# Kernel optimization log

Hardware: AMD Instinct MI355X
Metric: run time of the kernel (lower is better)

Reference implementation:

```python
import jax, jax.numpy as jnp
import numpy as np

N_HEAD = 8
DROP_RATE = 0.1


def setup_inputs() -> dict:
    key = jax.random.key(0)
    k1, k2, k3 = jax.random.split(key, 3)
    n, c, h, w = 16, 512, 32, 32
    return {
        "x": jax.random.normal(k1, (n, c, h, w), jnp.float32),
        "qkv_w": jax.random.normal(k2, (3 * c, c), jnp.float32) * 0.02,
        "qkv_b": jnp.zeros((3 * c,), jnp.float32),
        "out_w": jax.random.normal(k3, (c, c), jnp.float32) * 0.02,
        "out_b": jnp.zeros((c,), jnp.float32),
        "dropout_enabled": 0,
    }


def reference(x, qkv_w, qkv_b, out_w, out_b, dropout_enabled):
    n, c, h, w = x.shape
    hd = c // N_HEAD  # head dim
    # fused QKV 1x1 conv == per-pixel matmul: [n, 3c, h, w]
    qkv = jnp.einsum('oc,nchw->nohw', qkv_w, x) + qkv_b[None, :, None, None]
    # [n, 3*n_head, hd, h*w] -> [n, 3*n_head, h*w, hd]
    qkv = jnp.swapaxes(qkv.reshape(n, N_HEAD * 3, hd, h * w), 2, 3)
    q, k, v = jnp.split(qkv, 3, axis=1)  # each [n, n_head, hw, hd]
    scale = hd ** (-0.25)
    att = jax.nn.softmax((q * scale) @ (jnp.swapaxes(k, 2, 3) * scale), axis=3)
    y = jnp.swapaxes(att @ v, 2, 3).reshape(n, c, h, w)
    y = jnp.einsum('oc,nchw->nohw', out_w, y) + out_b[None, :, None, None]
    # Dropout2d: drops whole (n, c) channel maps
    rate = DROP_RATE * dropout_enabled
    keep = jax.random.bernoulli(jax.random.key(42), 1.0 - rate, shape=(n, c))
    y = y * keep[..., None, None] / (1.0 - rate)
    return x + y
```

## Files before the change

kernel.cpp:

```cpp
#include <hip/hip_runtime.h>

typedef short bf16x8 __attribute__((ext_vector_type(8)));
typedef float f32x4 __attribute__((ext_vector_type(4)));
typedef float f32x16 __attribute__((ext_vector_type(16)));

#define MFMA16(a,b,c) __builtin_amdgcn_mfma_f32_16x16x32_bf16((a),(b),(c),0,0,0)
#define MFMA32(a,b,c) __builtin_amdgcn_mfma_f32_32x32x16_bf16((a),(b),(c),0,0,0)

static __device__ __forceinline__ unsigned short f2bf(float f){
  unsigned u; __builtin_memcpy(&u, &f, 4);
  u += 0x7fffu + ((u >> 16) & 1u);
  return (unsigned short)(u >> 16);
}

static __device__ __forceinline__ unsigned cvtpk(float lo, float hi){
  unsigned r;
  asm volatile("v_cvt_pk_bf16_f32 %0, %1, %2" : "=v"(r) : "v"(lo), "v"(hi));
  return r;
}
static __device__ __forceinline__ void pl32swap(unsigned &a, unsigned &b){
  asm volatile("v_permlane32_swap_b32 %0, %1" : "+v"(a), "+v"(b));
}

static __device__ __forceinline__ void gload_lds16(const void* g, void* l) {
  __builtin_amdgcn_global_load_lds(
      (__attribute__((address_space(1))) void*)g,
      (__attribute__((address_space(3))) void*)l, 16, 0, 0);
}

__global__ __launch_bounds__(256) void cvt_w(
    const float* __restrict__ qkv_w, const float* __restrict__ out_w,
    unsigned short* __restrict__ wq, unsigned short* __restrict__ wo) {
  int i = blockIdx.x * 256 + threadIdx.x;
  if (i < 786432) wq[i] = f2bf(qkv_w[i]);
  else            wo[i - 786432] = f2bf(out_w[i - 786432]);
}

__global__ __launch_bounds__(256) void transpose_cvt(
    const float* __restrict__ in, unsigned short* __restrict__ out)
{
  __shared__ unsigned short tile[32][33];
  const long base = (long)blockIdx.z * 512 * 1024;
  const int t = threadIdx.x, tx = t & 31, ty = t >> 5;
  const int c0 = blockIdx.x * 32, r0 = blockIdx.y * 32;
  const float* ib = in + base;
#pragma unroll
  for (int i = 0; i < 4; ++i)
    tile[ty + i * 8][tx] = f2bf(ib[(long)(r0 + ty + i * 8) * 1024 + c0 + tx]);
  __syncthreads();
  unsigned short* ob = out + base;
#pragma unroll
  for (int i = 0; i < 4; ++i)
    ob[(long)(c0 + ty + i * 8) * 512 + r0 + tx] = tile[tx][ty + i * 8];
}

__global__ __launch_bounds__(256, 2) void gemm_qkv(
    const unsigned short* __restrict__ A, const unsigned short* __restrict__ B,
    unsigned short* __restrict__ qkvout, const float* __restrict__ bias)
{
  const int M = 1024, K = 512;
  __shared__ unsigned short SM[4][128 * 64];
  const int t = threadIdx.x, lane = t & 63, wv = t >> 6;
  const int quad = lane >> 4, ln = lane & 15;

  const int L = blockIdx.x + 12 * blockIdx.y + 96 * blockIdx.z;
  const int v = (L & 7) * 192 + (L >> 3);
  const int m0 = ((v / 12) & 7) * 128, n0 = (v % 12) * 128;
  const long zb = v / 96;
  A += zb * (long)M * K;

  const int srow = wv * 32 + (lane >> 3);
  const int scol = ((lane & 7) * 8) ^ ((lane >> 3) * 8);

  auto stage = [&](int kt, unsigned short* Ad, unsigned short* Bd) {
#pragma unroll
    for (int i = 0; i < 4; ++i) {
      gload_lds16(&A[(long)(m0 + srow + i * 8) * K + kt + scol],
                  &Ad[(wv * 32 + i * 8) * 64]);
      gload_lds16(&B[(long)(n0 + srow + i * 8) * K + kt + scol],
                  &Bd[(wv * 32 + i * 8) * 64]);
    }
  };

  f32x4 zero = {0.f, 0.f, 0.f, 0.f};
  f32x4 acc[4][4];
#pragma unroll
  for (int i = 0; i < 4; ++i)
#pragma unroll
    for (int j = 0; j < 4; ++j) acc[i][j] = zero;

  const int wm = (wv & 1) * 64, wn = (wv >> 1) * 64;
  const int rsw = (ln & 7) * 8;

  stage(0, SM[0], SM[2]);
  __syncthreads();
  for (int kt8 = 0; kt8 < 8; ++kt8) {
    const int cur = kt8 & 1;
    if (kt8 < 7) stage((kt8 + 1) * 64, SM[cur ^ 1], SM[2 + (cur ^ 1)]);
    const unsigned short* As = SM[cur];
    const unsigned short* Bs = SM[2 + cur];
#pragma unroll
    for (int kk = 0; kk < 64; kk += 32) {
      bf16x8 a[4], b[4];
#pragma unroll
      for (int i = 0; i < 4; ++i)
        a[i] = *(const bf16x8*)&As[(wm + i * 16 + ln) * 64 + ((kk + quad * 8) ^ rsw)];
#pragma unroll
      for (int j = 0; j < 4; ++j)
        b[j] = *(const bf16x8*)&Bs[(wn + j * 16 + ln) * 64 + ((kk + quad * 8) ^ rsw)];
#pragma unroll
      for (int i = 0; i < 4; ++i)
#pragma unroll
        for (int j = 0; j < 4; ++j)
          acc[i][j] = MFMA16(a[i], b[j], acc[i][j]);
    }
    __syncthreads();
  }

  const int part = n0 >> 9;
  if (part < 2) {
    const float qs = (part == 0) ? 0.18033688f : 1.0f;
    unsigned short (*T)[136] = (unsigned short(*)[136])&SM[0][0];
#pragma unroll
    for (int j = 0; j < 4; ++j) {
      const int oo = wn + j * 16 + ln;
      const float bb = bias[n0 + oo];
#pragma unroll
      for (int i = 0; i < 4; ++i) {
        const int pp = wm + i * 16 + quad * 4;
        f32x4 vv = acc[i][j];
#pragma unroll
        for (int r = 0; r < 4; ++r)
          T[pp + r][oo] = f2bf((vv[r] + bb) * qs);
      }
    }
    __syncthreads();
    unsigned short* qb = qkvout + (long)part * 8388608;
#pragma unroll
    for (int it = 0; it < 8; ++it) {
      const int idx = it * 256 + t;
      const int p = idx >> 4, c0 = (idx & 15) * 8;
      const int og = n0 + c0;
      const int h = (og >> 6) & 7, d = og & 63;
      bf16x8 val = *(const bf16x8*)&T[p][c0];
      *(bf16x8*)&qb[((long)(zb * 8 + h) * 1024 + m0 + p) * 64 + d] = val;
    }
  } else {
#pragma unroll
    for (int j = 0; j < 4; ++j) {
      const int o = n0 + wn + j * 16 + ln;
      const float bb = bias[o];
#pragma unroll
      for (int i = 0; i < 4; ++i) {
        const int p = m0 + wm + i * 16 + quad * 4;
        const long cidx = ((long)zb * 512 + (o - 1024)) * 1024 + p;
        f32x4 vv = acc[i][j];
        ushort4 st;
        st.x = f2bf(vv[0] + bb); st.y = f2bf(vv[1] + bb);
        st.z = f2bf(vv[2] + bb); st.w = f2bf(vv[3] + bb);
        *(ushort4*)&qkvout[16777216 + cidx] = st;
      }
    }
  }
}

__global__ __launch_bounds__(256, 2) void gemm_out(
    const unsigned short* __restrict__ A, const unsigned short* __restrict__ B,
    float* __restrict__ C, const float* __restrict__ bias,
    const float* __restrict__ xin, const int* __restrict__ de_ptr)
{
  const int M = 1024, K = 512;
  __shared__ unsigned short SM[4][128 * 64];
  const int t = threadIdx.x, lane = t & 63, wv = t >> 6;
  const int quad = lane >> 4, ln = lane & 15;

  const int L = blockIdx.x + 4 * blockIdx.y + 32 * blockIdx.z;
  const int v = (L & 7) * 64 + (L >> 3);
  const int m0 = ((v >> 2) & 7) * 128, n0 = (v & 3) * 128;
  const long zb = v >> 5;
  A += zb * (long)M * K;
  C += zb * 512l * M;
  xin += zb * 512l * M;

  const int srow = wv * 32 + (lane >> 3);
  const int scol = ((lane & 7) * 8) ^ ((lane >> 3) * 8);

  auto stage = [&](int kt, unsigned short* Ad, unsigned short* Bd) {
#pragma unroll
    for (int i = 0; i < 4; ++i) {
      gload_lds16(&A[(long)(m0 + srow + i * 8) * K + kt + scol],
                  &Ad[(wv * 32 + i * 8) * 64]);
      gload_lds16(&B[(long)(n0 + srow + i * 8) * K + kt + scol],
                  &Bd[(wv * 32 + i * 8) * 64]);
    }
  };

  f32x4 zero = {0.f, 0.f, 0.f, 0.f};
  f32x4 acc[4][4];
#pragma unroll
  for (int i = 0; i < 4; ++i)
#pragma unroll
    for (int j = 0; j < 4; ++j) acc[i][j] = zero;

  const int wm = (wv & 1) * 64, wn = (wv >> 1) * 64;
  const int rsw = (ln & 7) * 8;

  stage(0, SM[0], SM[2]);
  __syncthreads();
  for (int kt8 = 0; kt8 < 8; ++kt8) {
    const int cur = kt8 & 1;
    if (kt8 < 7) stage((kt8 + 1) * 64, SM[cur ^ 1], SM[2 + (cur ^ 1)]);
    const unsigned short* As = SM[cur];
    const unsigned short* Bs = SM[2 + cur];
#pragma unroll
    for (int kk = 0; kk < 64; kk += 32) {
      bf16x8 a[4], b[4];
#pragma unroll
      for (int i = 0; i < 4; ++i)
        a[i] = *(const bf16x8*)&As[(wm + i * 16 + ln) * 64 + ((kk + quad * 8) ^ rsw)];
#pragma unroll
      for (int j = 0; j < 4; ++j)
        b[j] = *(const bf16x8*)&Bs[(wn + j * 16 + ln) * 64 + ((kk + quad * 8) ^ rsw)];
#pragma unroll
      for (int i = 0; i < 4; ++i)
#pragma unroll
        for (int j = 0; j < 4; ++j)
          acc[i][j] = MFMA16(a[i], b[j], acc[i][j]);
    }
    __syncthreads();
  }

  float dscale = 1.0f / (1.0f - 0.1f * (float)de_ptr[0]);

#pragma unroll
  for (int j = 0; j < 4; ++j) {
    int o = n0 + wn + j * 16 + ln;
    float bb = bias[o];
#pragma unroll
    for (int i = 0; i < 4; ++i) {
      int p = m0 + wm + i * 16 + quad * 4;
      long cidx = (long)o * M + p;
      f32x4 vv = acc[i][j];
      float4 rx = *(const float4*)&xin[cidx];
      float4 st;
      st.x = rx.x + (vv[0] + bb) * dscale;
      st.y = rx.y + (vv[1] + bb) * dscale;
      st.z = rx.z + (vv[2] + bb) * dscale;
      st.w = rx.w + (vv[3] + bb) * dscale;
      *(float4*)&C[cidx] = st;
    }
  }
}

__global__ __launch_bounds__(512, 2) void attn_kernel(
    const unsigned short* __restrict__ q_pd, const unsigned short* __restrict__ k_pd,
    const unsigned short* __restrict__ v_cp, unsigned short* __restrict__ y_pc)
{
  __shared__ unsigned short Ks[2][128 * 64];
  __shared__ unsigned short Vs[2][64 * 128];
  const int t = threadIdx.x, lane = t & 63, wv = t >> 6;
  const int l31 = lane & 31, bh8 = (lane >> 5) * 8;
  const int qt = blockIdx.y >> 5;
  const int nh = blockIdx.x * 32 + (blockIdx.y & 31);
  const int n = nh >> 3, h = nh & 7;
  const int q0 = qt * 512;

  bf16x8 qa[2][4];
#pragma unroll
  for (int qg = 0; qg < 2; ++qg) {
    const unsigned short* qb =
        q_pd + ((long)nh * 1024 + q0 + wv * 64 + qg * 32 + l31) * 64;
#pragma unroll
    for (int ds = 0; ds < 4; ++ds)
      qa[qg][ds] = *(const bf16x8*)(qb + ds * 16 + bh8);
  }

  f32x16 zacc;
#pragma unroll
  for (int r = 0; r < 16; ++r) zacc[r] = 0.f;
  f32x16 o_acc[2][2];
  o_acc[0][0] = zacc; o_acc[0][1] = zacc; o_acc[1][0] = zacc; o_acc[1][1] = zacc;
  float l_acc[2] = {0.f, 0.f};

  const unsigned short* kg0 = k_pd + (long)nh * 1024 * 64;
  const unsigned short* vg0 = v_cp + ((long)n * 512 + h * 64) * 1024;

  const int krow = lane >> 3;
  const int kcol = ((lane & 7) * 8) ^ ((lane >> 3) * 8);
  const int vrow = lane >> 4;
  const int rsw = (lane & 7) * 8;
  const int vrsw = (l31 & 15) * 8;

  auto stage_kv = [&](int c, int buf) {
    const unsigned short* kg = kg0 + (long)c * 128 * 64;
    const unsigned short* vg = vg0 + c * 128;
    unsigned short* KsD = Ks[buf];
    unsigned short* VsD = Vs[buf];
#pragma unroll
    for (int i = 0; i < 2; ++i) {
      const int vr = ((wv & 1) * 8) + i * 4 + vrow;
      const int vcol = ((lane & 15) ^ vr) * 8;
      gload_lds16(kg + (long)(wv * 16 + i * 8 + krow) * 64 + kcol,
                  &KsD[(wv * 16 + i * 8) * 64]);
      gload_lds16(vg + (long)(wv * 8 + i * 4 + vrow) * 1024 + vcol,
                  &VsD[(wv * 8 + i * 4) * 128]);
    }
  };

  stage_kv(0, 0);

  union U { bf16x8 v; unsigned u[4]; };
  auto sm_pack = [&](const f32x16& sv, bf16x8* paq, float& lac) {
    float e[16];
#pragma unroll
    for (int r = 0; r < 16; ++r) e[r] = __builtin_amdgcn_exp2f(sv[r]);
    float a0 = e[0] + e[1],  a1 = e[2] + e[3],  a2 = e[4] + e[5],  a3 = e[6] + e[7];
    float a4 = e[8] + e[9],  a5 = e[10] + e[11], a6 = e[12] + e[13], a7 = e[14] + e[15];
    float b0 = a0 + a1, b1 = a2 + a3, b2 = a4 + a5, b3 = a6 + a7;
    lac += (b0 + b1) + (b2 + b3);
    unsigned pk4[4][2];
#pragma unroll
    for (int hh = 0; hh < 4; ++hh) {
      pk4[hh][0] = cvtpk(e[4 * hh + 0], e[4 * hh + 1]);
      pk4[hh][1] = cvtpk(e[4 * hh + 2], e[4 * hh + 3]);
    }
#pragma unroll
    for (int hk = 0; hk < 2; ++hk) {
      unsigned x0 = pk4[2 * hk + 1][0], y0 = pk4[2 * hk][0];
      unsigned x1 = pk4[2 * hk + 1][1], y1 = pk4[2 * hk][1];
      pl32swap(x0, y0); pl32swap(x1, y1);
      U u; u.u[0] = y0; u.u[1] = y1; u.u[2] = x0; u.u[3] = x1;
      paq[hk] = u.v;
    }
  };

  for (int c = 0; c < 8; ++c) {
    const int cur = c & 1;
    if (c < 7) {
      stage_kv(c + 1, cur ^ 1);
      asm volatile("s_waitcnt vmcnt(4)" ::: "memory");
    } else {
      asm volatile("s_waitcnt vmcnt(0)" ::: "memory");
    }
    __builtin_amdgcn_s_barrier();
    const unsigned short* KsC = Ks[cur];
    const unsigned short* VsC = Vs[cur];

#pragma unroll
    for (int g = 0; g < 2; ++g) {
      bf16x8 ka[2][4];
#pragma unroll
      for (int kk = 0; kk < 2; ++kk)
#pragma unroll
        for (int ds = 0; ds < 4; ++ds)
          ka[kk][ds] = *(const bf16x8*)
              &KsC[((g * 2 + kk) * 32 + l31) * 64 + ((ds * 16 + bh8) ^ rsw)];
      f32x16 s[2][2];
      s[0][0] = zacc; s[0][1] = zacc; s[1][0] = zacc; s[1][1] = zacc;
      __builtin_amdgcn_s_setprio(1);
#pragma unroll
      for (int ds = 0; ds < 4; ++ds)
#pragma unroll
        for (int kk = 0; kk < 2; ++kk) {
          s[kk][0] = MFMA32(ka[kk][ds], qa[0][ds], s[kk][0]);
          s[kk][1] = MFMA32(ka[kk][ds], qa[1][ds], s[kk][1]);
        }
      __builtin_amdgcn_s_setprio(0);
#pragma unroll
      for (int kk = 0; kk < 2; ++kk) {
        bf16x8 va[4];
#pragma unroll
        for (int dg = 0; dg < 2; ++dg)
#pragma unroll
          for (int hk = 0; hk < 2; ++hk)
            va[dg * 2 + hk] = *(const bf16x8*)
                &VsC[(dg * 32 + l31) * 128 + ((((g * 2 + kk) * 2 + hk) * 16 + bh8) ^ vrsw)];
        bf16x8 pa[2][2];
        sm_pack(s[kk][0], pa[0], l_acc[0]);
        sm_pack(s[kk][1], pa[1], l_acc[1]);
        __builtin_amdgcn_s_setprio(1);
#pragma unroll
        for (int dg = 0; dg < 2; ++dg)
#pragma unroll
          for (int hk = 0; hk < 2; ++hk) {
            o_acc[dg][0] = MFMA32(va[dg * 2 + hk], pa[0][hk], o_acc[dg][0]);
            o_acc[dg][1] = MFMA32(va[dg * 2 + hk], pa[1][hk], o_acc[dg][1]);
          }
        __builtin_amdgcn_s_setprio(0);
      }
    }
    __builtin_amdgcn_s_barrier();
  }

#pragma unroll
  for (int qg = 0; qg < 2; ++qg) {
    float la = l_acc[qg];
    la += __shfl_xor(la, 32);
    float linv = 1.0f / la;
    const int q = q0 + wv * 64 + qg * 32 + l31;
    unsigned short* yb = y_pc + ((long)n * 1024 + q) * 512 + h * 64;
#pragma unroll
    for (int dg = 0; dg < 2; ++dg) {
      f32x16 o = o_acc[dg][qg];
#pragma unroll
      for (int rq = 0; rq < 4; ++rq) {
        int d0 = dg * 32 + rq * 8 + (bh8 >> 1);
        ushort4 st;
        st.x = f2bf(o[rq * 4 + 0] * linv);
        st.y = f2bf(o[rq * 4 + 1] * linv);
        st.z = f2bf(o[rq * 4 + 2] * linv);
        st.w = f2bf(o[rq * 4 + 3] * linv);
        *(ushort4*)&yb[d0] = st;
      }
    }
  }
}

extern "C" void kernel_launch(void* const* d_in, const int* in_sizes, int n_in,
                              void* d_out, int out_size, void* d_ws, size_t ws_size,
                              hipStream_t stream) {
  (void)in_sizes; (void)n_in; (void)out_size; (void)ws_size;
  const float* x     = (const float*)d_in[0];
  const float* qkv_w = (const float*)d_in[1];
  const float* qkv_b = (const float*)d_in[2];
  const float* out_w = (const float*)d_in[3];
  const float* out_b = (const float*)d_in[4];
  const int* de = (const int*)d_in[5];
  float* out = (float*)d_out;
  unsigned short* ws = (unsigned short*)d_ws;

  unsigned short* xT   = ws;
  unsigned short* qkv  = ws + 8388608;
  unsigned short* y_pc = ws;
  unsigned short* wq   = ws + 33554432;
  unsigned short* wo   = wq + 786432;

  cvt_w<<<4096, 256, 0, stream>>>(qkv_w, out_w, wq, wo);

  transpose_cvt<<<dim3(32, 16, 16), 256, 0, stream>>>(x, xT);

  gemm_qkv<<<dim3(12, 8, 16), 256, 0, stream>>>(xT, wq, qkv, qkv_b);

  attn_kernel<<<dim3(4, 64), 512, 0, stream>>>(
      qkv, qkv + 8388608, qkv + 16777216, y_pc);

  gemm_out<<<dim3(4, 8, 16), 256, 0, stream>>>(
      y_pc, wo, out, out_b, x, de);
}
```

Baseline: 199.8 us.

## Software-pipeline QK and PV MFMAs in attention; fuse weight cvt into transpose

The attention inner loop is restructured so that the QK^T MFMAs for the next 32-key group are issued before the softmax/pack and PV MFMAs of the current group, using ping-pong score registers. This overlaps the softmax VALU work with matrix-core work. Separately, the weight bf16 conversion kernel is merged into the transpose kernel as extra blocks, removing one launch and vectorising the conversion to float2 loads. The pipelining raises register pressure, with two sets of score accumulators live at once.

```diff
diff --git a/kernel.cpp b/kernel.cpp
--- a/kernel.cpp
+++ b/kernel.cpp
@@ -28,18 +28,21 @@
       (__attribute__((address_space(3))) void*)l, 16, 0, 0);
 }
 
-__global__ __launch_bounds__(256) void cvt_w(
+__global__ __launch_bounds__(256) void transpose_cvt(
+    const float* __restrict__ in, unsigned short* __restrict__ out,
     const float* __restrict__ qkv_w, const float* __restrict__ out_w,
-    unsigned short* __restrict__ wq, unsigned short* __restrict__ wo) {
-  int i = blockIdx.x * 256 + threadIdx.x;
-  if (i < 786432) wq[i] = f2bf(qkv_w[i]);
-  else            wo[i - 786432] = f2bf(out_w[i - 786432]);
-}
-
-__global__ __launch_bounds__(256) void transpose_cvt(
-    const float* __restrict__ in, unsigned short* __restrict__ out)
+    unsigned short* __restrict__ wq, unsigned short* __restrict__ wo)
 {
   __shared__ unsigned short tile[32][33];
+  if (blockIdx.x >= 32) {
+    const int b = (blockIdx.x - 32) + 8 * (blockIdx.y + 16 * blockIdx.z);
+    const int i = b * 512 + threadIdx.x * 2;
+    float2 v; unsigned short* dst;
+    if (i < 786432) { v = *(const float2*)&qkv_w[i]; dst = &wq[i]; }
+    else { v = *(const float2*)&out_w[i - 786432]; dst = &wo[i - 786432]; }
+    dst[0] = f2bf(v.x); dst[1] = f2bf(v.y);
+    return;
+  }
   const long base = (long)blockIdx.z * 512 * 1024;
   const int t = threadIdx.x, tx = t & 31, ty = t >> 5;
   const int c0 = blockIdx.x * 32, r0 = blockIdx.y * 32;
@@ -334,6 +337,46 @@
     }
   };
 
+  auto qk_issue = [&](const unsigned short* KsC, int kgi, f32x16* s) {
+    bf16x8 ka[4];
+#pragma unroll
+    for (int ds = 0; ds < 4; ++ds)
+      ka[ds] = *(const bf16x8*)
+          &KsC[(kgi * 32 + l31) * 64 + ((ds * 16 + bh8) ^ rsw)];
+    s[0] = zacc; s[1] = zacc;
+    __builtin_amdgcn_s_setprio(1);
+#pragma unroll
+    for (int ds = 0; ds < 4; ++ds) {
+      s[0] = MFMA32(ka[ds], qa[0][ds], s[0]);
+      s[1] = MFMA32(ka[ds], qa[1][ds], s[1]);
+    }
+    __builtin_amdgcn_s_setprio(0);
+  };
+
+  auto body = [&](const unsigned short* KsC, const unsigned short* VsC,
+                  int kgi, f32x16* scur, f32x16* snxt) {
+    if (kgi < 3) qk_issue(KsC, kgi + 1, snxt);
+    bf16x8 va[4];
+#pragma unroll
+    for (int dg = 0; dg < 2; ++dg)
+#pragma unroll
+      for (int hk = 0; hk < 2; ++hk)
+        va[dg * 2 + hk] = *(const bf16x8*)
+            &VsC[(dg * 32 + l31) * 128 + (((kgi * 2 + hk) * 16 + bh8) ^ vrsw)];
+    bf16x8 pa[2][2];
+    sm_pack(scur[0], pa[0], l_acc[0]);
+    sm_pack(scur[1], pa[1], l_acc[1]);
+    __builtin_amdgcn_s_setprio(1);
+#pragma unroll
+    for (int dg = 0; dg < 2; ++dg)
+#pragma unroll
+      for (int hk = 0; hk < 2; ++hk) {
+        o_acc[dg][0] = MFMA32(va[dg * 2 + hk], pa[0][hk], o_acc[dg][0]);
+        o_acc[dg][1] = MFMA32(va[dg * 2 + hk], pa[1][hk], o_acc[dg][1]);
+      }
+    __builtin_amdgcn_s_setprio(0);
+  };
+
   for (int c = 0; c < 8; ++c) {
     const int cur = c & 1;
     if (c < 7) {
@@ -346,49 +389,13 @@
     const unsigned short* KsC = Ks[cur];
     const unsigned short* VsC = Vs[cur];
 
-#pragma unroll
-    for (int g = 0; g < 2; ++g) {
-      bf16x8 ka[2][4];
-#pragma unroll
-      for (int kk = 0; kk < 2; ++kk)
-#pragma unroll
-        for (int ds = 0; ds < 4; ++ds)
-          ka[kk][ds] = *(const bf16x8*)
-              &KsC[((g * 2 + kk) * 32 + l31) * 64 + ((ds * 16 + bh8) ^ rsw)];
-      f32x16 s[2][2];
-      s[0][0] = zacc; s[0][1] = zacc; s[1][0] = zacc; s[1][1] = zacc;
-      __builtin_amdgcn_s_setprio(1);
-#pragma unroll
-      for (int ds = 0; ds < 4; ++ds)
-#pragma unroll
-        for (int kk = 0; kk < 2; ++kk) {
-          s[kk][0] = MFMA32(ka[kk][ds], qa[0][ds], s[kk][0]);
-          s[kk][1] = MFMA32(ka[kk][ds], qa[1][ds], s[kk][1]);
-        }
-      __builtin_amdgcn_s_setprio(0);
-#pragma unroll
-      for (int kk = 0; kk < 2; ++kk) {
-        bf16x8 va[4];
-#pragma unroll
-        for (int dg = 0; dg < 2; ++dg)
-#pragma unroll
-          for (int hk = 0; hk < 2; ++hk)
-            va[dg * 2 + hk] = *(const bf16x8*)
-                &VsC[(dg * 32 + l31) * 128 + ((((g * 2 + kk) * 2 + hk) * 16 + bh8) ^ vrsw)];
-        bf16x8 pa[2][2];
-        sm_pack(s[kk][0], pa[0], l_acc[0]);
-        sm_pack(s[kk][1], pa[1], l_acc[1]);
-        __builtin_amdgcn_s_setprio(1);
-#pragma unroll
-        for (int dg = 0; dg < 2; ++dg)
-#pragma unroll
-          for (int hk = 0; hk < 2; ++hk) {
-            o_acc[dg][0] = MFMA32(va[dg * 2 + hk], pa[0][hk], o_acc[dg][0]);
-            o_acc[dg][1] = MFMA32(va[dg * 2 + hk], pa[1][hk], o_acc[dg][1]);
-          }
-        __builtin_amdgcn_s_setprio(0);
-      }
-    }
+    f32x16 sA[2], sB[2];
+    qk_issue(KsC, 0, sA);
+    body(KsC, VsC, 0, sA, sB);
+    body(KsC, VsC, 1, sB, sA);
+    body(KsC, VsC, 2, sA, sB);
+    body(KsC, VsC, 3, sB, sA);
+
     __builtin_amdgcn_s_barrier();
   }
 
@@ -435,9 +442,8 @@
   unsigned short* wq   = ws + 33554432;
   unsigned short* wo   = wq + 786432;
 
-  cvt_w<<<4096, 256, 0, stream>>>(qkv_w, out_w, wq, wo);
-
-  transpose_cvt<<<dim3(32, 16, 16), 256, 0, stream>>>(x, xT);
+  transpose_cvt<<<dim3(40, 16, 16), 256, 0, stream>>>(
+      x, xT, qkv_w, out_w, wq, wo);
 
   gemm_qkv<<<dim3(12, 8, 16), 256, 0, stream>>>(xT, wq, qkv, qkv_b);
 
```

Result: faster. 181.8 us (-9.0%).
